# Kernel optimization log

Measured on AMD Instinct MI355X. Metric: run time of the kernel, lower is better.

The kernel has to match this reference:

```python
import jax, jax.numpy as jnp
import numpy as np

N_NODES = 100000
N_EDGES = 1600000
IN_CH = 64
HIDDEN = 64
OUT_CH = 32
MAX_VEL = 0.9  # max_relative_velocity (fraction of c)
EPS = 1e-6


def _glorot(key, shape):
    fan_in, fan_out = shape
    lim = (6.0 / (fan_in + fan_out)) ** 0.5
    return jax.random.uniform(key, shape, jnp.float32, -lim, lim)


def setup_inputs() -> dict:
    key = jax.random.key(0)
    k_x, k_e, k_w1, k_w2 = jax.random.split(key, 4)
    x = jax.random.normal(k_x, (N_NODES, IN_CH), jnp.float32)
    edge_index = jax.random.randint(k_e, (2, N_EDGES), 0, N_NODES, jnp.int32)
    W1 = _glorot(k_w1, (IN_CH, HIDDEN))
    b1 = jnp.zeros((HIDDEN,), jnp.float32)
    W2 = _glorot(k_w2, (HIDDEN, OUT_CH))
    b2 = jnp.zeros((OUT_CH,), jnp.float32)
    return {"x": x, "edge_index": edge_index, "W1": W1, "b1": b1, "W2": W2, "b2": b2}


def rel_graph_conv(x, edge_index, W, b):
    """RelativisticGraphConv: linear transform + velocity-weighted message passing.

    Per-edge relative velocity v = tanh(||x_src - x_dst||) * max_vel (< c),
    Lorentz factor gamma = 1/sqrt(1 - v^2); messages attenuated by time
    dilation 1/gamma, scatter-summed into destination nodes, degree-normalized.
    """
    src, dst = edge_index[0], edge_index[1]
    h = x @ W + b                                     # [N, out]
    diff = x[src] - x[dst]                            # [E, in] (edge gather)
    v = jnp.tanh(jnp.linalg.norm(diff, axis=-1)) * MAX_VEL   # [E]
    gamma = 1.0 / jnp.sqrt(1.0 - v * v + EPS)
    w = 1.0 / gamma                                   # time-dilation weight in (0,1]
    msg = h[src] * w[:, None]                         # [E, out]
    agg = jax.ops.segment_sum(msg, dst, num_segments=N_NODES)
    deg = jax.ops.segment_sum(jnp.ones_like(w), dst, num_segments=N_NODES)
    return agg / jnp.clip(deg, 1.0)[:, None]


def reference(x, edge_index, W1, b1, W2, b2):
    h = rel_graph_conv(x, edge_index, W1, b1)
    h = jax.nn.relu(h)
    # dropout is identity in eval mode (training=False)
    out = rel_graph_conv(h, edge_index, W2, b2)
    return out
```

## Files before the change

kernel.cpp:

```cpp
#include <hip/hip_runtime.h>
#include <hip/hip_fp16.h>
#include <math.h>

#define MAX_VEL 0.9f
#define REL_EPS 1e-6f

#define BSH 8
#define BSZ 256
#define BCAP 5120

typedef int v4i __attribute__((ext_vector_type(4)));

__device__ __forceinline__ float lorentz_w(float sq)
{
    float r  = __builtin_amdgcn_sqrtf(sq);
    float E  = __builtin_amdgcn_exp2f(r * 2.8853900817779268f);
    float ip = __builtin_amdgcn_rcpf(E + 1.0f);
    float th = fmaf(-2.0f, ip, 1.0f);
    return __builtin_amdgcn_sqrtf(fmaf(-(MAX_VEL * MAX_VEL), th * th, 1.0f + REL_EPS));
}

__device__ __forceinline__ float group16_sum(float v)
{
    int t;
    t = __builtin_amdgcn_update_dpp(0, __float_as_int(v), 0xB1, 0xF, 0xF, true);
    v += __int_as_float(t);
    t = __builtin_amdgcn_update_dpp(0, __float_as_int(v), 0x4E, 0xF, 0xF, true);
    v += __int_as_float(t);
    t = __builtin_amdgcn_update_dpp(0, __float_as_int(v), 0x141, 0xF, 0xF, true);
    v += __int_as_float(t);
    t = __builtin_amdgcn_update_dpp(0, __float_as_int(v), 0x140, 0xF, 0xF, true);
    v += __int_as_float(t);
    return v;
}

__global__ void cvt_zero(const float* __restrict__ in, __half2* __restrict__ out, int n4,
                         int* __restrict__ bcnt, int nbuk)
{
    int i = blockIdx.x * blockDim.x + threadIdx.x;
    if (i < nbuk) bcnt[i] = 0;
    if (i >= n4) return;
    float4 v = reinterpret_cast<const float4*>(in)[i];
    float2 lo; lo.x = v.x; lo.y = v.y;
    float2 hi; hi.x = v.z; hi.y = v.w;
    out[2 * i]     = __float22half2_rn(lo);
    out[2 * i + 1] = __float22half2_rn(hi);
}

#define A_TPB 1024
#define A_EPT 16
#define A_EPB (A_TPB * A_EPT)
__global__ __launch_bounds__(1024) void passA(
    const int* __restrict__ src, const int* __restrict__ dst,
    int* __restrict__ bcnt, unsigned int* __restrict__ bbuf, int E, int nbuk)
{
    __shared__ int lhist[512];
    __shared__ int lbase[512];
    __shared__ int lcur[512];
    int t = threadIdx.x;
    if (t < 512) { lhist[t] = 0; lcur[t] = 0; }
    __syncthreads();
    int base0 = blockIdx.x * A_EPB;

    for (int i = 0; i < A_EPT; ++i) {
        int e = base0 + i * A_TPB + t;
        if (e < E) {
            int d = __builtin_nontemporal_load(dst + e);
            atomicAdd(&lhist[d >> BSH], 1);
        }
    }
    __syncthreads();

    if (t < nbuk) lbase[t] = (lhist[t] > 0) ? atomicAdd(&bcnt[t], lhist[t]) : 0;
    __syncthreads();

    for (int i = 0; i < A_EPT; ++i) {
        int e = base0 + i * A_TPB + t;
        if (e < E) {
            int d = __builtin_nontemporal_load(dst + e);
            int s = __builtin_nontemporal_load(src + e);
            int b = d >> BSH;
            int idx = atomicAdd(&lcur[b], 1);
            int pos = lbase[b] + idx;
            if (pos < BCAP)
                bbuf[(size_t)b * BCAP + pos] = ((unsigned)s << BSH) | (unsigned)(d & (BSZ - 1));
        }
    }
}

__global__ __launch_bounds__(512) void scan_buckets(const int* __restrict__ bcnt,
                                                    int* __restrict__ bboff, int nbuk)
{
    __shared__ int s[512];
    int t = threadIdx.x;
    int v = (t < nbuk) ? bcnt[t] : 0;
    s[t] = v;
    __syncthreads();
    for (int off = 1; off < 512; off <<= 1) {
        int a = (t >= off) ? s[t - off] : 0;
        __syncthreads();
        s[t] += a;
        __syncthreads();
    }
    if (t < nbuk) bboff[t] = s[t] - v;
}

__global__ __launch_bounds__(256) void passB(
    const unsigned int* __restrict__ bbuf, const int* __restrict__ bcnt,
    const int* __restrict__ bboff,
    int* __restrict__ cnt, int* __restrict__ cursor,
    int* __restrict__ src_sorted, int N)
{
    __shared__ int lcnt[256];
    __shared__ int lrp[256];
    __shared__ int lex[256];
    __shared__ int lcur[256];
    int b = blockIdx.x;
    int t = threadIdx.x;
    lcnt[t] = 0;
    lcur[t] = 0;
    __syncthreads();

    int n = bcnt[b];
    n = n < BCAP ? n : BCAP;
    const unsigned int* bb = bbuf + (size_t)b * BCAP;

    for (int i = t; i < n; i += 256)
        atomicAdd(&lcnt[bb[i] & (BSZ - 1)], 1);
    __syncthreads();

    lrp[t] = lcnt[t];
    __syncthreads();
    for (int off = 1; off < 256; off <<= 1) {
        int a = (t >= off) ? lrp[t - off] : 0;
        __syncthreads();
        lrp[t] += a;
        __syncthreads();
    }
    lex[t] = lrp[t] - lcnt[t];
    __syncthreads();

    int bo = bboff[b];
    int node = b * BSZ + t;
    if (node < N) {
        cnt[node] = lcnt[t];
        cursor[node] = bo + lex[t];
    }

    for (int i = t; i < n; i += 256) {
        unsigned p = bb[i];
        int dl = p & (BSZ - 1);
        int r = atomicAdd(&lcur[dl], 1);
        src_sorted[bo + lex[dl] + r] = (int)(p >> BSH);
    }
}

__device__ __forceinline__ float4 load_h4(const __half* Fh, size_t off)
{
    uint2 u = *reinterpret_cast<const uint2*>(Fh + off);
    float2 lo = __half22float2(*reinterpret_cast<const __half2*>(&u.x));
    float2 hi = __half22float2(*reinterpret_cast<const __half2*>(&u.y));
    float4 f;
    f.x = lo.x; f.y = lo.y; f.z = hi.x; f.w = hi.y;
    return f;
}

#define AGG_BODY(fK, swA, axA, ayA, azA, awA)                                        \
    {                                                                                \
        float dx = fK.x - fd.x, dy = fK.y - fd.y, dz = fK.z - fd.z, dw = fK.w - fd.w;\
        float sq = dx * dx;                                                          \
        sq = fmaf(dy, dy, sq);                                                       \
        sq = fmaf(dz, dz, sq);                                                       \
        sq = fmaf(dw, dw, sq);                                                       \
        sq = group16_sum(sq);                                                        \
        float w = lorentz_w(sq);                                                     \
        swA += w;                                                                    \
        axA = fmaf(fK.x, w, axA);                                                    \
        ayA = fmaf(fK.y, w, ayA);                                                    \
        azA = fmaf(fK.z, w, azA);                                                    \
        awA = fmaf(fK.w, w, awA);                                                    \
    }

__global__ void agg_pass_h(const __half* __restrict__ Fh, const int* __restrict__ cursor,
                           const int* __restrict__ cnt, const int* __restrict__ src_sorted,
                           __half* __restrict__ aggh, float* __restrict__ sumw, int N)
{
    int node = (blockIdx.x * blockDim.x + threadIdx.x) >> 4;
    int gl = threadIdx.x & 15;
    int gl4 = gl * 4;
    if (node >= N) return;
    int deg = cnt[node];
    int beg = cursor[node];
    int end = beg + deg;
    float4 fd = load_h4(Fh, (size_t)node * 64 + gl4);
    float ax0 = 0.f, ay0 = 0.f, az0 = 0.f, aw0 = 0.f, sw0 = 0.f;
    float ax1 = 0.f, ay1 = 0.f, az1 = 0.f, aw1 = 0.f, sw1 = 0.f;
    int p = beg;
    for (; p + 8 <= end; p += 8) {
        int s0 = src_sorted[p];
        int s1 = src_sorted[p + 1];
        int s2 = src_sorted[p + 2];
        int s3 = src_sorted[p + 3];
        int s4 = src_sorted[p + 4];
        int s5 = src_sorted[p + 5];
        int s6 = src_sorted[p + 6];
        int s7 = src_sorted[p + 7];
        float4 f0 = load_h4(Fh, (size_t)s0 * 64 + gl4);
        float4 f1 = load_h4(Fh, (size_t)s1 * 64 + gl4);
        float4 f2 = load_h4(Fh, (size_t)s2 * 64 + gl4);
        float4 f3 = load_h4(Fh, (size_t)s3 * 64 + gl4);
        float4 f4 = load_h4(Fh, (size_t)s4 * 64 + gl4);
        float4 f5 = load_h4(Fh, (size_t)s5 * 64 + gl4);
        float4 f6 = load_h4(Fh, (size_t)s6 * 64 + gl4);
        float4 f7 = load_h4(Fh, (size_t)s7 * 64 + gl4);
        AGG_BODY(f0, sw0, ax0, ay0, az0, aw0)
        AGG_BODY(f1, sw1, ax1, ay1, az1, aw1)
        AGG_BODY(f2, sw0, ax0, ay0, az0, aw0)
        AGG_BODY(f3, sw1, ax1, ay1, az1, aw1)
        AGG_BODY(f4, sw0, ax0, ay0, az0, aw0)
        AGG_BODY(f5, sw1, ax1, ay1, az1, aw1)
        AGG_BODY(f6, sw0, ax0, ay0, az0, aw0)
        AGG_BODY(f7, sw1, ax1, ay1, az1, aw1)
    }
    for (; p + 4 <= end; p += 4) {
        int s0 = src_sorted[p];
        int s1 = src_sorted[p + 1];
        int s2 = src_sorted[p + 2];
        int s3 = src_sorted[p + 3];
        float4 f0 = load_h4(Fh, (size_t)s0 * 64 + gl4);
        float4 f1 = load_h4(Fh, (size_t)s1 * 64 + gl4);
        float4 f2 = load_h4(Fh, (size_t)s2 * 64 + gl4);
        float4 f3 = load_h4(Fh, (size_t)s3 * 64 + gl4);
        AGG_BODY(f0, sw0, ax0, ay0, az0, aw0)
        AGG_BODY(f1, sw1, ax1, ay1, az1, aw1)
        AGG_BODY(f2, sw0, ax0, ay0, az0, aw0)
        AGG_BODY(f3, sw1, ax1, ay1, az1, aw1)
    }
    for (; p < end; ++p) {
        int s0 = src_sorted[p];
        float4 f0 = load_h4(Fh, (size_t)s0 * 64 + gl4);
        AGG_BODY(f0, sw0, ax0, ay0, az0, aw0)
    }
    float2 lo, hi;
    lo.x = ax0 + ax1;
    lo.y = ay0 + ay1;
    hi.x = az0 + az1;
    hi.y = aw0 + aw1;
    uint2 u;
    *reinterpret_cast<__half2*>(&u.x) = __float22half2_rn(lo);
    *reinterpret_cast<__half2*>(&u.y) = __float22half2_rn(hi);
    *reinterpret_cast<uint2*>(aggh + (size_t)node * 64 + gl4) = u;
    if (gl == 0) sumw[node] = sw0 + sw1;
}

__device__ __forceinline__ float4 cvt_lo(uint4 h)
{
    float2 a = __half22float2(*reinterpret_cast<const __half2*>(&h.x));
    float2 b = __half22float2(*reinterpret_cast<const __half2*>(&h.y));
    float4 f; f.x = a.x; f.y = a.y; f.z = b.x; f.w = b.y;
    return f;
}
__device__ __forceinline__ float4 cvt_hi(uint4 h)
{
    float2 a = __half22float2(*reinterpret_cast<const __half2*>(&h.z));
    float2 b = __half22float2(*reinterpret_cast<const __half2*>(&h.w));
    float4 f; f.x = a.x; f.y = a.y; f.z = b.x; f.w = b.y;
    return f;
}

#define LIN_FMA4(i)                                   \
    a0 = fmaf(r##i.x, wreg[4 * i + 0], a0);           \
    a1 = fmaf(r##i.y, wreg[4 * i + 1], a1);           \
    a2 = fmaf(r##i.z, wreg[4 * i + 2], a2);           \
    a3 = fmaf(r##i.w, wreg[4 * i + 3], a3);

__global__ __launch_bounds__(256) void lin1_post(
    const __half* __restrict__ agghb, const float* __restrict__ W1,
    const float* __restrict__ b1, const float* __restrict__ sumw,
    const int* __restrict__ cnt, __half* __restrict__ hiddenh, int N)
{
    int c = threadIdx.x & 63;
    float wreg[64];
#pragma unroll
    for (int k = 0; k < 64; ++k) wreg[k] = W1[k * 64 + c];
    float bc = b1[c];
    int sub = threadIdx.x >> 6;
    for (int node = blockIdx.x * 4 + sub; node < N; node += gridDim.x * 4) {
        const uint4* hr = reinterpret_cast<const uint4*>(agghb + (size_t)node * 64);
        uint4 h0 = hr[0], h1 = hr[1], h2 = hr[2], h3 = hr[3];
        uint4 h4 = hr[4], h5 = hr[5], h6 = hr[6], h7 = hr[7];
        int dg = cnt[node];
        float sw = sumw[node];
        float4 r0 = cvt_lo(h0), r1 = cvt_hi(h0), r2 = cvt_lo(h1), r3 = cvt_hi(h1);
        float4 r4 = cvt_lo(h2), r5 = cvt_hi(h2), r6 = cvt_lo(h3), r7 = cvt_hi(h3);
        float4 r8 = cvt_lo(h4), r9 = cvt_hi(h4), r10 = cvt_lo(h5), r11 = cvt_hi(h5);
        float4 r12 = cvt_lo(h6), r13 = cvt_hi(h6), r14 = cvt_lo(h7), r15 = cvt_hi(h7);
        float a0 = 0.f, a1 = 0.f, a2 = 0.f, a3 = 0.f;
        LIN_FMA4(0)  LIN_FMA4(1)  LIN_FMA4(2)  LIN_FMA4(3)
        LIN_FMA4(4)  LIN_FMA4(5)  LIN_FMA4(6)  LIN_FMA4(7)
        LIN_FMA4(8)  LIN_FMA4(9)  LIN_FMA4(10) LIN_FMA4(11)
        LIN_FMA4(12) LIN_FMA4(13) LIN_FMA4(14) LIN_FMA4(15)
        float acc = (a0 + a1) + (a2 + a3);
        float inv = 1.0f / (dg > 1 ? (float)dg : 1.0f);
        float val = (acc + bc * sw) * inv;
        hiddenh[(size_t)node * 64 + c] = __float2half_rn(fmaxf(val, 0.0f));
    }
}

__global__ __launch_bounds__(256) void lin2_post(
    const __half* __restrict__ agghb, const float* __restrict__ W2,
    const float* __restrict__ b2, const float* __restrict__ sumw,
    const int* __restrict__ cnt, float* __restrict__ out, int N)
{
    int c = threadIdx.x & 31;
    float wreg[64];
#pragma unroll
    for (int k = 0; k < 64; ++k) wreg[k] = W2[k * 32 + c];
    float bc = b2[c];
    int sub = threadIdx.x >> 5;
    for (int node = blockIdx.x * 8 + sub; node < N; node += gridDim.x * 8) {
        const uint4* hr = reinterpret_cast<const uint4*>(agghb + (size_t)node * 64);
        uint4 h0 = hr[0], h1 = hr[1], h2 = hr[2], h3 = hr[3];
        uint4 h4 = hr[4], h5 = hr[5], h6 = hr[6], h7 = hr[7];
        int dg = cnt[node];
        float sw = sumw[node];
        float4 r0 = cvt_lo(h0), r1 = cvt_hi(h0), r2 = cvt_lo(h1), r3 = cvt_hi(h1);
        float4 r4 = cvt_lo(h2), r5 = cvt_hi(h2), r6 = cvt_lo(h3), r7 = cvt_hi(h3);
        float4 r8 = cvt_lo(h4), r9 = cvt_hi(h4), r10 = cvt_lo(h5), r11 = cvt_hi(h5);
        float4 r12 = cvt_lo(h6), r13 = cvt_hi(h6), r14 = cvt_lo(h7), r15 = cvt_hi(h7);
        float a0 = 0.f, a1 = 0.f, a2 = 0.f, a3 = 0.f;
        LIN_FMA4(0)  LIN_FMA4(1)  LIN_FMA4(2)  LIN_FMA4(3)
        LIN_FMA4(4)  LIN_FMA4(5)  LIN_FMA4(6)  LIN_FMA4(7)
        LIN_FMA4(8)  LIN_FMA4(9)  LIN_FMA4(10) LIN_FMA4(11)
        LIN_FMA4(12) LIN_FMA4(13) LIN_FMA4(14) LIN_FMA4(15)
        float acc = (a0 + a1) + (a2 + a3);
        float inv = 1.0f / (dg > 1 ? (float)dg : 1.0f);
        out[(size_t)node * 32 + c] = (acc + bc * sw) * inv;
    }
}

extern "C" void kernel_launch(void* const* d_in, const int* in_sizes, int n_in,
                              void* d_out, int out_size, void* d_ws, size_t ws_size,
                              hipStream_t stream)
{
    const float* x  = (const float*)d_in[0];
    const int*   ei = (const int*)d_in[1];
    const float* W1 = (const float*)d_in[2];
    const float* b1 = (const float*)d_in[3];
    const float* W2 = (const float*)d_in[4];
    const float* b2 = (const float*)d_in[5];
    float* out = (float*)d_out;

    const int N = in_sizes[0] / 64;
    const int E = in_sizes[1] / 2;
    const int* src = ei;
    const int* dst = ei + E;
    const int nbuk = (N + BSZ - 1) / BSZ;

    float*  ws      = (float*)d_ws;
    __half* aggh    = (__half*)ws;
    __half* xh      = (__half*)((float*)ws + (size_t)N * 32);
    __half* hiddenh = (__half*)((float*)xh + (size_t)N * 32);
    float*  sumw    = (float*)hiddenh + (size_t)N * 32;
    int*    cnt     = (int*)(sumw + N);
    int*    cursor  = cnt + N;
    int*    bcnt    = cursor + N;
    int*    bboff   = bcnt + 512;
    int*    src_sorted = bboff + 512;
    unsigned int* bbuf = (unsigned int*)aggh;

    int n4 = N * 16;
    cvt_zero<<<(n4 + 255) / 256, 256, 0, stream>>>(x, (__half2*)xh, n4, bcnt, nbuk);

    int ablk = (E + A_EPB - 1) / A_EPB;
    passA<<<ablk, A_TPB, 0, stream>>>(src, dst, bcnt, bbuf, E, nbuk);

    scan_buckets<<<1, 512, 0, stream>>>(bcnt, bboff, nbuk);

    passB<<<nbuk, 256, 0, stream>>>(bbuf, bcnt, bboff, cnt, cursor, src_sorted, N);

    int gblk = (int)(((size_t)N * 16 + 255) / 256);
    agg_pass_h<<<gblk, 256, 0, stream>>>(xh, cursor, cnt, src_sorted, aggh, sumw, N);
    lin1_post<<<2048, 256, 0, stream>>>(aggh, W1, b1, sumw, cnt, hiddenh, N);

    agg_pass_h<<<gblk, 256, 0, stream>>>(hiddenh, cursor, cnt, src_sorted, aggh, sumw, N);
    lin2_post<<<2048, 256, 0, stream>>>(aggh, W2, b2, sumw, cnt, out, N);
}
```

Baseline: 205.0 us.

## Use 8 lanes per node with 16-byte loads and packed fp16 dot2 distances

Each node in the aggregation kernel is now handled by 8 lanes instead of 16. Each lane loads 8 halfs at once as a 16-byte load, computes the squared distance with packed fp16 subtraction and fdot2, and reduces across the group with one fewer DPP step. This halves the per-edge lorentz weight computation and the index loads per node and widens the memory transactions. In exchange, the subtraction now happens in fp16, which costs precision, there are fewer threads per node, and each lane holds more registers.

```diff
diff --git a/kernel.cpp b/kernel.cpp
--- a/kernel.cpp
+++ b/kernel.cpp
@@ -10,6 +10,13 @@
 #define BCAP 5120
 
 typedef int v4i __attribute__((ext_vector_type(4)));
+typedef _Float16 v2h __attribute__((ext_vector_type(2)));
+
+#if __has_builtin(__builtin_amdgcn_fdot2)
+#define DOT2(a, b, c) __builtin_amdgcn_fdot2((a), (b), (c), false)
+#else
+#define DOT2(a, b, c) fmaf((float)(a).x, (float)(b).x, fmaf((float)(a).y, (float)(b).y, (c)))
+#endif
 
 __device__ __forceinline__ float lorentz_w(float sq)
 {
@@ -20,7 +27,7 @@
     return __builtin_amdgcn_sqrtf(fmaf(-(MAX_VEL * MAX_VEL), th * th, 1.0f + REL_EPS));
 }
 
-__device__ __forceinline__ float group16_sum(float v)
+__device__ __forceinline__ float group8_sum(float v)
 {
     int t;
     t = __builtin_amdgcn_update_dpp(0, __float_as_int(v), 0xB1, 0xF, 0xF, true);
@@ -28,8 +35,6 @@
     t = __builtin_amdgcn_update_dpp(0, __float_as_int(v), 0x4E, 0xF, 0xF, true);
     v += __int_as_float(t);
     t = __builtin_amdgcn_update_dpp(0, __float_as_int(v), 0x141, 0xF, 0xF, true);
-    v += __int_as_float(t);
-    t = __builtin_amdgcn_update_dpp(0, __float_as_int(v), 0x140, 0xF, 0xF, true);
     v += __int_as_float(t);
     return v;
 }
@@ -70,10 +75,8 @@
         }
     }
     __syncthreads();
-
     if (t < nbuk) lbase[t] = (lhist[t] > 0) ? atomicAdd(&bcnt[t], lhist[t]) : 0;
     __syncthreads();
-
     for (int i = 0; i < A_EPT; ++i) {
         int e = base0 + i * A_TPB + t;
         if (e < E) {
@@ -155,46 +158,43 @@
     }
 }
 
-__device__ __forceinline__ float4 load_h4(const __half* Fh, size_t off)
-{
-    uint2 u = *reinterpret_cast<const uint2*>(Fh + off);
-    float2 lo = __half22float2(*reinterpret_cast<const __half2*>(&u.x));
-    float2 hi = __half22float2(*reinterpret_cast<const __half2*>(&u.y));
-    float4 f;
-    f.x = lo.x; f.y = lo.y; f.z = hi.x; f.w = hi.y;
-    return f;
-}
-
-#define AGG_BODY(fK, swA, axA, ayA, azA, awA)                                        \
-    {                                                                                \
-        float dx = fK.x - fd.x, dy = fK.y - fd.y, dz = fK.z - fd.z, dw = fK.w - fd.w;\
-        float sq = dx * dx;                                                          \
-        sq = fmaf(dy, dy, sq);                                                       \
-        sq = fmaf(dz, dz, sq);                                                       \
-        sq = fmaf(dw, dw, sq);                                                       \
-        sq = group16_sum(sq);                                                        \
-        float w = lorentz_w(sq);                                                     \
-        swA += w;                                                                    \
-        axA = fmaf(fK.x, w, axA);                                                    \
-        ayA = fmaf(fK.y, w, ayA);                                                    \
-        azA = fmaf(fK.z, w, azA);                                                    \
-        awA = fmaf(fK.w, w, awA);                                                    \
+#define AGG8_BODY(fK)                                                       \
+    {                                                                       \
+        v2h* hk = reinterpret_cast<v2h*>(&fK);                              \
+        v2h d0 = hk[0] - hd0;                                               \
+        v2h d1 = hk[1] - hd1;                                               \
+        v2h d2 = hk[2] - hd2;                                               \
+        v2h d3 = hk[3] - hd3;                                               \
+        float sq = DOT2(d0, d0, DOT2(d1, d1, DOT2(d2, d2, DOT2(d3, d3, 0.0f)))); \
+        sq = group8_sum(sq);                                                \
+        float w = lorentz_w(sq);                                            \
+        sw += w;                                                            \
+        a0 = fmaf((float)hk[0].x, w, a0);                                   \
+        a1 = fmaf((float)hk[0].y, w, a1);                                   \
+        a2 = fmaf((float)hk[1].x, w, a2);                                   \
+        a3 = fmaf((float)hk[1].y, w, a3);                                   \
+        a4 = fmaf((float)hk[2].x, w, a4);                                   \
+        a5 = fmaf((float)hk[2].y, w, a5);                                   \
+        a6 = fmaf((float)hk[3].x, w, a6);                                   \
+        a7 = fmaf((float)hk[3].y, w, a7);                                   \
     }
 
 __global__ void agg_pass_h(const __half* __restrict__ Fh, const int* __restrict__ cursor,
                            const int* __restrict__ cnt, const int* __restrict__ src_sorted,
                            __half* __restrict__ aggh, float* __restrict__ sumw, int N)
 {
-    int node = (blockIdx.x * blockDim.x + threadIdx.x) >> 4;
-    int gl = threadIdx.x & 15;
-    int gl4 = gl * 4;
+    int node = (blockIdx.x * blockDim.x + threadIdx.x) >> 3;
+    int gl = threadIdx.x & 7;
+    int gl8 = gl * 8;
     if (node >= N) return;
     int deg = cnt[node];
     int beg = cursor[node];
     int end = beg + deg;
-    float4 fd = load_h4(Fh, (size_t)node * 64 + gl4);
-    float ax0 = 0.f, ay0 = 0.f, az0 = 0.f, aw0 = 0.f, sw0 = 0.f;
-    float ax1 = 0.f, ay1 = 0.f, az1 = 0.f, aw1 = 0.f, sw1 = 0.f;
+    uint4 fdv = *reinterpret_cast<const uint4*>(Fh + (size_t)node * 64 + gl8);
+    v2h* hdp = reinterpret_cast<v2h*>(&fdv);
+    v2h hd0 = hdp[0], hd1 = hdp[1], hd2 = hdp[2], hd3 = hdp[3];
+    float a0 = 0.f, a1 = 0.f, a2 = 0.f, a3 = 0.f;
+    float a4 = 0.f, a5 = 0.f, a6 = 0.f, a7 = 0.f, sw = 0.f;
     int p = beg;
     for (; p + 8 <= end; p += 8) {
         int s0 = src_sorted[p];
@@ -205,52 +205,52 @@
         int s5 = src_sorted[p + 5];
         int s6 = src_sorted[p + 6];
         int s7 = src_sorted[p + 7];
-        float4 f0 = load_h4(Fh, (size_t)s0 * 64 + gl4);
-        float4 f1 = load_h4(Fh, (size_t)s1 * 64 + gl4);
-        float4 f2 = load_h4(Fh, (size_t)s2 * 64 + gl4);
-        float4 f3 = load_h4(Fh, (size_t)s3 * 64 + gl4);
-        float4 f4 = load_h4(Fh, (size_t)s4 * 64 + gl4);
-        float4 f5 = load_h4(Fh, (size_t)s5 * 64 + gl4);
-        float4 f6 = load_h4(Fh, (size_t)s6 * 64 + gl4);
-        float4 f7 = load_h4(Fh, (size_t)s7 * 64 + gl4);
-        AGG_BODY(f0, sw0, ax0, ay0, az0, aw0)
-        AGG_BODY(f1, sw1, ax1, ay1, az1, aw1)
-        AGG_BODY(f2, sw0, ax0, ay0, az0, aw0)
-        AGG_BODY(f3, sw1, ax1, ay1, az1, aw1)
-        AGG_BODY(f4, sw0, ax0, ay0, az0, aw0)
-        AGG_BODY(f5, sw1, ax1, ay1, az1, aw1)
-        AGG_BODY(f6, sw0, ax0, ay0, az0, aw0)
-        AGG_BODY(f7, sw1, ax1, ay1, az1, aw1)
+        uint4 f0 = *reinterpret_cast<const uint4*>(Fh + (size_t)s0 * 64 + gl8);
+        uint4 f1 = *reinterpret_cast<const uint4*>(Fh + (size_t)s1 * 64 + gl8);
+        uint4 f2 = *reinterpret_cast<const uint4*>(Fh + (size_t)s2 * 64 + gl8);
+        uint4 f3 = *reinterpret_cast<const uint4*>(Fh + (size_t)s3 * 64 + gl8);
+        uint4 f4 = *reinterpret_cast<const uint4*>(Fh + (size_t)s4 * 64 + gl8);
+        uint4 f5 = *reinterpret_cast<const uint4*>(Fh + (size_t)s5 * 64 + gl8);
+        uint4 f6 = *reinterpret_cast<const uint4*>(Fh + (size_t)s6 * 64 + gl8);
+        uint4 f7 = *reinterpret_cast<const uint4*>(Fh + (size_t)s7 * 64 + gl8);
+        AGG8_BODY(f0)
+        AGG8_BODY(f1)
+        AGG8_BODY(f2)
+        AGG8_BODY(f3)
+        AGG8_BODY(f4)
+        AGG8_BODY(f5)
+        AGG8_BODY(f6)
+        AGG8_BODY(f7)
     }
     for (; p + 4 <= end; p += 4) {
         int s0 = src_sorted[p];
         int s1 = src_sorted[p + 1];
         int s2 = src_sorted[p + 2];
         int s3 = src_sorted[p + 3];
-        float4 f0 = load_h4(Fh, (size_t)s0 * 64 + gl4);
-        float4 f1 = load_h4(Fh, (size_t)s1 * 64 + gl4);
-        float4 f2 = load_h4(Fh, (size_t)s2 * 64 + gl4);
-        float4 f3 = load_h4(Fh, (size_t)s3 * 64 + gl4);
-        AGG_BODY(f0, sw0, ax0, ay0, az0, aw0)
-        AGG_BODY(f1, sw1, ax1, ay1, az1, aw1)
-        AGG_BODY(f2, sw0, ax0, ay0, az0, aw0)
-        AGG_BODY(f3, sw1, ax1, ay1, az1, aw1)
+        uint4 f0 = *reinterpret_cast<const uint4*>(Fh + (size_t)s0 * 64 + gl8);
+        uint4 f1 = *reinterpret_cast<const uint4*>(Fh + (size_t)s1 * 64 + gl8);
+        uint4 f2 = *reinterpret_cast<const uint4*>(Fh + (size_t)s2 * 64 + gl8);
+        uint4 f3 = *reinterpret_cast<const uint4*>(Fh + (size_t)s3 * 64 + gl8);
+        AGG8_BODY(f0)
+        AGG8_BODY(f1)
+        AGG8_BODY(f2)
+        AGG8_BODY(f3)
     }
     for (; p < end; ++p) {
         int s0 = src_sorted[p];
-        float4 f0 = load_h4(Fh, (size_t)s0 * 64 + gl4);
-        AGG_BODY(f0, sw0, ax0, ay0, az0, aw0)
-    }
-    float2 lo, hi;
-    lo.x = ax0 + ax1;
-    lo.y = ay0 + ay1;
-    hi.x = az0 + az1;
-    hi.y = aw0 + aw1;
-    uint2 u;
-    *reinterpret_cast<__half2*>(&u.x) = __float22half2_rn(lo);
-    *reinterpret_cast<__half2*>(&u.y) = __float22half2_rn(hi);
-    *reinterpret_cast<uint2*>(aggh + (size_t)node * 64 + gl4) = u;
-    if (gl == 0) sumw[node] = sw0 + sw1;
+        uint4 f0 = *reinterpret_cast<const uint4*>(Fh + (size_t)s0 * 64 + gl8);
+        AGG8_BODY(f0)
+    }
+    uint4 o;
+    v2h* op = reinterpret_cast<v2h*>(&o);
+    v2h r0, r1, r2, r3;
+    r0.x = (_Float16)a0; r0.y = (_Float16)a1;
+    r1.x = (_Float16)a2; r1.y = (_Float16)a3;
+    r2.x = (_Float16)a4; r2.y = (_Float16)a5;
+    r3.x = (_Float16)a6; r3.y = (_Float16)a7;
+    op[0] = r0; op[1] = r1; op[2] = r2; op[3] = r3;
+    *reinterpret_cast<uint4*>(aggh + (size_t)node * 64 + gl8) = o;
+    if (gl == 0) sumw[node] = sw;
 }
 
 __device__ __forceinline__ float4 cvt_lo(uint4 h)
@@ -379,7 +379,7 @@
 
     passB<<<nbuk, 256, 0, stream>>>(bbuf, bcnt, bboff, cnt, cursor, src_sorted, N);
 
-    int gblk = (int)(((size_t)N * 16 + 255) / 256);
+    int gblk = (int)(((size_t)N * 8 + 255) / 256);
     agg_pass_h<<<gblk, 256, 0, stream>>>(xh, cursor, cnt, src_sorted, aggh, sumw, N);
     lin1_post<<<2048, 256, 0, stream>>>(aggh, W1, b1, sumw, cnt, hiddenh, N);
 
```

Measured after the change: 193.3 us. -5.7%, faster.
